# Performance work log

Measured on AMD Instinct MI355X. Metric: run time of the kernel, lower is better.

Reference implementation:

```python
import jax, jax.numpy as jnp
import numpy as np

N_NODES = 100000
N_EDGES = 1000000
IN_DIM = 64
OUT_DIM = 64
BN_EPS = 1e-5


def setup_inputs() -> dict:
    key = jax.random.key(0)
    k1, k2, k3 = jax.random.split(key, 3)
    x = jax.random.normal(k1, (N_NODES, IN_DIM), dtype=jnp.float32)
    edge_index = jax.random.randint(k2, (2, N_EDGES), 0, N_NODES, dtype=jnp.int32)
    W = jax.random.normal(k3, (IN_DIM, OUT_DIM), dtype=jnp.float32) * (1.0 / np.sqrt(IN_DIM))
    b = jnp.zeros((OUT_DIM,), dtype=jnp.float32)
    gamma = jnp.ones((OUT_DIM,), dtype=jnp.float32)
    beta = jnp.zeros((OUT_DIM,), dtype=jnp.float32)
    return {"x": x, "edge_index": edge_index, "W": W, "b": b, "gamma": gamma, "beta": beta}


def reference(x, edge_index, W, b, gamma, beta):
    N = x.shape[0]
    # GCN normalization with self-loops (improved=False -> fill value 1.0)
    loop = jnp.arange(N, dtype=edge_index.dtype)
    src = jnp.concatenate([edge_index[0], loop])  # message sources
    dst = jnp.concatenate([edge_index[1], loop])  # aggregation targets
    ew = jnp.ones(src.shape[0], dtype=x.dtype)
    deg = jax.ops.segment_sum(ew, dst, num_segments=N)  # [N]
    dinv = jnp.where(deg > 0, jax.lax.rsqrt(deg), 0.0)
    norm = dinv[src] * ew * dinv[dst]  # [E+N]
    # linear transform then normalized scatter-add aggregation
    h = x @ W  # [N, OUT_DIM]
    msg = h[src] * norm[:, None]  # [E+N, OUT_DIM]
    agg = jax.ops.segment_sum(msg, dst, num_segments=N) + b  # [N, OUT_DIM]
    # activation
    a = jax.nn.relu(agg)
    # BatchNorm1d, training mode: batch statistics over node dim (biased var)
    mean = jnp.mean(a, axis=0)
    var = jnp.mean((a - mean) ** 2, axis=0)
    out = gamma * (a - mean) * jax.lax.rsqrt(var + BN_EPS) + beta
    return out
```

## Files before the change

### kernel.cpp

```cpp
#include <hip/hip_runtime.h>
#include <hip/hip_fp16.h>

#define DIM 64
#define BN_EPS 1e-5f
#define RSHIFT 8
#define RSIZE 256
#define EPB 8192
#define SBLK 512

__global__ __launch_bounds__(256) void k_binhist(const int* __restrict__ dst,
                                                 int* __restrict__ rangecnt,
                                                 int P, int E) {
    __shared__ int hist[512];
    for (int b = threadIdx.x; b < P; b += 256) hist[b] = 0;
    __syncthreads();
    const int base4 = blockIdx.x * (EPB / 4);
    for (int i = 0; i < EPB / 4 / 256; ++i) {
        int idx = base4 + i * 256 + threadIdx.x;
        int e0 = idx << 2;
        if (e0 + 3 < E) {
            int4 d4 = ((const int4*)dst)[idx];
            atomicAdd(&hist[d4.x >> RSHIFT], 1);
            atomicAdd(&hist[d4.y >> RSHIFT], 1);
            atomicAdd(&hist[d4.z >> RSHIFT], 1);
            atomicAdd(&hist[d4.w >> RSHIFT], 1);
        } else {
            for (int k = 0; k < 4; ++k)
                if (e0 + k < E) atomicAdd(&hist[dst[e0 + k] >> RSHIFT], 1);
        }
    }
    __syncthreads();
    for (int b = threadIdx.x; b < P; b += 256)
        if (hist[b] > 0) atomicAdd(&rangecnt[b], hist[b]);
}

__global__ void k_rangescan(const int* __restrict__ rangecnt, int* __restrict__ gbase,
                            int* __restrict__ gcursor, int* __restrict__ rowptr,
                            int P, int N, int E) {
    __shared__ int s[512];
    int v = ((int)threadIdx.x < P) ? rangecnt[threadIdx.x] : 0;
    s[threadIdx.x] = v;
    __syncthreads();
    for (int off = 1; off < 512; off <<= 1) {
        int t = (threadIdx.x >= (unsigned)off) ? s[threadIdx.x - off] : 0;
        __syncthreads();
        s[threadIdx.x] += t;
        __syncthreads();
    }
    if ((int)threadIdx.x < P) {
        int ex = s[threadIdx.x] - v;
        gbase[threadIdx.x] = ex;
        gcursor[threadIdx.x] = ex;
    }
    if ((int)threadIdx.x == P - 1) gbase[P] = s[threadIdx.x];
    if (threadIdx.x == 0) rowptr[N] = E;
}

__global__ __launch_bounds__(256) void k_bin(const int* __restrict__ src,
                                             const int* __restrict__ dst,
                                             int* __restrict__ gcursor,
                                             int* __restrict__ pk, int P, int E) {
    __shared__ int hist[512], gofs[512], lcnt[512];
    for (int b = threadIdx.x; b < P; b += 256) { hist[b] = 0; lcnt[b] = 0; }
    __syncthreads();
    const int base4 = blockIdx.x * (EPB / 4);
    for (int i = 0; i < EPB / 4 / 256; ++i) {
        int idx = base4 + i * 256 + threadIdx.x;
        int e0 = idx << 2;
        if (e0 + 3 < E) {
            int4 d4 = ((const int4*)dst)[idx];
            atomicAdd(&hist[d4.x >> RSHIFT], 1);
            atomicAdd(&hist[d4.y >> RSHIFT], 1);
            atomicAdd(&hist[d4.z >> RSHIFT], 1);
            atomicAdd(&hist[d4.w >> RSHIFT], 1);
        } else {
            for (int k = 0; k < 4; ++k)
                if (e0 + k < E) atomicAdd(&hist[dst[e0 + k] >> RSHIFT], 1);
        }
    }
    __syncthreads();
    for (int b = threadIdx.x; b < P; b += 256)
        if (hist[b] > 0) gofs[b] = atomicAdd(&gcursor[b], hist[b]);
    __syncthreads();
    for (int i = 0; i < EPB / 4 / 256; ++i) {
        int idx = base4 + i * 256 + threadIdx.x;
        int e0 = idx << 2;
        if (e0 + 3 < E) {
            int4 d4 = ((const int4*)dst)[idx];
            int4 s4 = ((const int4*)src)[idx];
            int b;
            b = d4.x >> RSHIFT; pk[gofs[b] + atomicAdd(&lcnt[b], 1)] = ((d4.x & (RSIZE - 1)) << 20) | s4.x;
            b = d4.y >> RSHIFT; pk[gofs[b] + atomicAdd(&lcnt[b], 1)] = ((d4.y & (RSIZE - 1)) << 20) | s4.y;
            b = d4.z >> RSHIFT; pk[gofs[b] + atomicAdd(&lcnt[b], 1)] = ((d4.z & (RSIZE - 1)) << 20) | s4.z;
            b = d4.w >> RSHIFT; pk[gofs[b] + atomicAdd(&lcnt[b], 1)] = ((d4.w & (RSIZE - 1)) << 20) | s4.w;
        } else {
            for (int k = 0; k < 4; ++k) {
                if (e0 + k < E) {
                    int d = dst[e0 + k];
                    int b = d >> RSHIFT;
                    pk[gofs[b] + atomicAdd(&lcnt[b], 1)] = ((d & (RSIZE - 1)) << 20) | src[e0 + k];
                }
            }
        }
    }
}

__global__ __launch_bounds__(256) void k_sortrange(
        const int* __restrict__ gbase, const int* __restrict__ pk,
        int* __restrict__ ssrc, int* __restrict__ rowptr,
        int* __restrict__ chunkstart, float* __restrict__ dinv, int N) {
    __shared__ int lhist[256], ls[256], lcur[256];
    const int r = blockIdx.x;
    const int d0 = r << RSHIFT;
    const int i = d0 + threadIdx.x;
    const int ebeg = gbase[r], eend = gbase[r + 1];
    lhist[threadIdx.x] = 0;
    __syncthreads();
    for (int j = ebeg + threadIdx.x; j < eend; j += 256)
        atomicAdd(&lhist[((unsigned)pk[j]) >> 20], 1);
    __syncthreads();
    int dg = lhist[threadIdx.x];
    if (i < N) dinv[i] = rsqrtf((float)dg + 1.0f);
    ls[threadIdx.x] = dg;
    __syncthreads();
    for (int off = 1; off < 256; off <<= 1) {
        int t = (threadIdx.x >= (unsigned)off) ? ls[threadIdx.x - off] : 0;
        __syncthreads();
        ls[threadIdx.x] += t;
        __syncthreads();
    }
    int lofs = ls[threadIdx.x] - dg;
    lcur[threadIdx.x] = ebeg + lofs;
    if (i < N) {
        int rs = ebeg + lofs;
        rowptr[i] = rs;
        int rn = rs + dg;
        int c0 = (rs + 63) >> 6;
        int c1 = (rn + 63) >> 6;
        for (int c = c0; c < c1; ++c) chunkstart[c] = i;
    }
    __syncthreads();
    for (int j = ebeg + threadIdx.x; j < eend; j += 256) {
        int p = pk[j];
        ssrc[atomicAdd(&lcur[((unsigned)p) >> 20], 1)] = p & 0xFFFFF;
    }
}

__global__ __launch_bounds__(256) void k_gemm(const float* __restrict__ x,
                                              const float* __restrict__ W,
                                              const float* __restrict__ dinv,
                                              __half* __restrict__ h2,
                                              float* __restrict__ outseed, int N) {
    __shared__ float Wl[DIM * DIM];
    for (int i = threadIdx.x; i < DIM * DIM; i += 256) Wl[i] = W[i];
    __syncthreads();
    int t = blockIdx.x * 256 + threadIdx.x;
    int r = t >> 2;
    int q = t & 3;
    if (r >= N) return;
    const float4* xr4 = (const float4*)(x + (size_t)r * DIM);
    float4 acc[4];
#pragma unroll
    for (int j = 0; j < 4; ++j) acc[j] = make_float4(0.f, 0.f, 0.f, 0.f);
    for (int k0 = 0; k0 < 16; ++k0) {
        float4 xv = xr4[k0];
#pragma unroll
        for (int kk = 0; kk < 4; ++kk) {
            float xs = (&xv.x)[kk];
            const float4* wrow = (const float4*)(Wl + (k0 * 4 + kk) * DIM) + (q << 2);
#pragma unroll
            for (int j = 0; j < 4; ++j) {
                float4 w = wrow[j];
                acc[j].x += xs * w.x;
                acc[j].y += xs * w.y;
                acc[j].z += xs * w.z;
                acc[j].w += xs * w.w;
            }
        }
    }
    float dr = dinv[r];
    float4* os4 = (float4*)(outseed + (size_t)r * DIM) + (q << 2);
    float4* hr4 = (float4*)(h2 + (size_t)r * DIM) + (q << 1);
    union { __half2 h[4]; float4 f4; } pack;
#pragma unroll
    for (int j = 0; j < 4; j += 2) {
        float4 v0 = make_float4(acc[j].x * dr, acc[j].y * dr, acc[j].z * dr, acc[j].w * dr);
        float4 v1 = make_float4(acc[j + 1].x * dr, acc[j + 1].y * dr, acc[j + 1].z * dr, acc[j + 1].w * dr);
        os4[j] = v0;
        os4[j + 1] = v1;
        pack.h[0] = __float22half2_rn(make_float2(v0.x, v0.y));
        pack.h[1] = __float22half2_rn(make_float2(v0.z, v0.w));
        pack.h[2] = __float22half2_rn(make_float2(v1.x, v1.y));
        pack.h[3] = __float22half2_rn(make_float2(v1.z, v1.w));
        hr4[j >> 1] = pack.f4;
    }
}

__global__ __launch_bounds__(256) void k_edgeagg(
        const int* __restrict__ ssrc, const int* __restrict__ rowptr,
        const int* __restrict__ chunkstart, const __half* __restrict__ h2,
        float* __restrict__ agg, int N, int E) {
    const int lane = threadIdx.x & 63;
    const int wid = blockIdx.x * (blockDim.x >> 6) + (threadIdx.x >> 6);
    const int base = wid << 6;
    if (base >= E) return;
    const int nval = min(64, E - base);
    const int node0 = chunkstart[wid];
    int sv = ssrc[base + min(lane, nval - 1)];
    int nn = node0 + 1 + lane;
    if (nn > N) nn = N;
    int rp = rowptr[nn];
    const __half* hb = h2 + lane;
    float acc = 0.f;
    bool uncovered = (__builtin_amdgcn_readlane(rp, 63) <= base + nval - 1);
    if (!uncovered && nval == 64) {
        int dprev = node0 + __popcll(__ballot(rp <= base));
#pragma unroll
        for (int g = 0; g < 64; g += 8) {
            int sA[8];
            float vA[8];
            int dA[8];
#pragma unroll
            for (int k = 0; k < 8; ++k) sA[k] = __builtin_amdgcn_readlane(sv, g + k);
#pragma unroll
            for (int k = 0; k < 8; ++k) vA[k] = __half2float(hb[(size_t)sA[k] * DIM]);
#pragma unroll
            for (int k = 0; k < 8; ++k) dA[k] = node0 + __popcll(__ballot(rp <= base + g + k));
#pragma unroll
            for (int k = 0; k < 8; ++k) {
                if (dA[k] != dprev) {
                    atomicAdd(&agg[(size_t)dprev * DIM + lane], acc);
                    acc = 0.f;
                    dprev = dA[k];
                }
                acc += vA[k];
            }
        }
        atomicAdd(&agg[(size_t)dprev * DIM + lane], acc);
    } else if (!uncovered) {
        int dprev = node0 + __popcll(__ballot(rp <= base));
        for (int j = 0; j < nval; ++j) {
            int sj = __builtin_amdgcn_readlane(sv, j);
            int dj = node0 + __popcll(__ballot(rp <= base + j));
            if (dj != dprev) {
                atomicAdd(&agg[(size_t)dprev * DIM + lane], acc);
                acc = 0.f;
                dprev = dj;
            }
            acc += __half2float(hb[(size_t)sj * DIM]);
        }
        atomicAdd(&agg[(size_t)dprev * DIM + lane], acc);
    } else {
        int dprev = -1;
        for (int j = 0; j < nval; ++j) {
            int e = base + j;
            int lo = 0, hi = N - 1;
            while (lo < hi) {
                int mid = (lo + hi + 1) >> 1;
                if (rowptr[mid] <= e) lo = mid; else hi = mid - 1;
            }
            if (lo != dprev) {
                if (dprev >= 0) atomicAdd(&agg[(size_t)dprev * DIM + lane], acc);
                acc = 0.f;
                dprev = lo;
            }
            acc += __half2float(hb[(size_t)__builtin_amdgcn_readlane(sv, j) * DIM]);
        }
        if (dprev >= 0) atomicAdd(&agg[(size_t)dprev * DIM + lane], acc);
    }
}

__global__ __launch_bounds__(256) void k_stats(
        const float4* __restrict__ outr, const float* __restrict__ dinv,
        const float* __restrict__ b, float* __restrict__ pstats, int total4) {
    __shared__ float4 s1[256], s2[256];
    int i = blockIdx.x * 256 + threadIdx.x;
    const int stride = SBLK * 256;
    const int f4 = i & 15;
    const float4 bv = ((const float4*)b)[f4];
    float4 ls = make_float4(0.f, 0.f, 0.f, 0.f), lq = ls;
    for (; i < total4; i += stride) {
        float dd = dinv[i >> 4];
        float4 v = outr[i];
        float ax = fmaxf(v.x * dd + bv.x, 0.f);
        float ay = fmaxf(v.y * dd + bv.y, 0.f);
        float az = fmaxf(v.z * dd + bv.z, 0.f);
        float aw = fmaxf(v.w * dd + bv.w, 0.f);
        ls.x += ax; ls.y += ay; ls.z += az; ls.w += aw;
        lq.x += ax * ax; lq.y += ay * ay; lq.z += az * az; lq.w += aw * aw;
    }
    s1[threadIdx.x] = ls;
    s2[threadIdx.x] = lq;
    __syncthreads();
    for (int o = 128; o >= 16; o >>= 1) {
        if ((int)threadIdx.x < o) {
            float4 a = s1[threadIdx.x], c = s1[threadIdx.x + o];
            s1[threadIdx.x] = make_float4(a.x + c.x, a.y + c.y, a.z + c.z, a.w + c.w);
            float4 q = s2[threadIdx.x], r = s2[threadIdx.x + o];
            s2[threadIdx.x] = make_float4(q.x + r.x, q.y + r.y, q.z + r.z, q.w + r.w);
        }
        __syncthreads();
    }
    if (threadIdx.x < 16) {
        ((float4*)(pstats + (size_t)blockIdx.x * 128))[threadIdx.x] = s1[threadIdx.x];
        ((float4*)(pstats + (size_t)blockIdx.x * 128 + 64))[threadIdx.x] = s2[threadIdx.x];
    }
}

__global__ void k_finstats(const float* __restrict__ pstats,
                           const float* __restrict__ gamma, const float* __restrict__ beta,
                           float* __restrict__ scale, float* __restrict__ shift, int N) {
    __shared__ float ssum[256], ssq[256];
    const int f = threadIdx.x & 63;
    const int c = threadIdx.x >> 6;
    float s = 0.f, q = 0.f;
    for (int blk = c; blk < SBLK; blk += 4) {
        s += pstats[blk * 128 + f];
        q += pstats[blk * 128 + 64 + f];
    }
    ssum[threadIdx.x] = s;
    ssq[threadIdx.x] = q;
    __syncthreads();
    if (threadIdx.x < 64) {
        float ts = ssum[f] + ssum[f + 64] + ssum[f + 128] + ssum[f + 192];
        float tq = ssq[f] + ssq[f + 64] + ssq[f + 128] + ssq[f + 192];
        float inv_n = 1.0f / (float)N;
        float mean = ts * inv_n;
        float var = tq * inv_n - mean * mean;
        float istd = rsqrtf(var + BN_EPS);
        float sc = gamma[f] * istd;
        scale[f] = sc;
        shift[f] = beta[f] - mean * sc;
    }
}

__global__ void k_bn2(float4* __restrict__ a, const float* __restrict__ dinv,
                      const float* __restrict__ b, const float* __restrict__ scale,
                      const float* __restrict__ shift, int total4) {
    int i = blockIdx.x * blockDim.x + threadIdx.x;
    const int stride = gridDim.x * blockDim.x;
    const int f4 = i & 15;
    const float4 bv = ((const float4*)b)[f4];
    const float4 scv = ((const float4*)scale)[f4];
    const float4 shv = ((const float4*)shift)[f4];
    for (; i < total4; i += stride) {
        float dd = dinv[i >> 4];
        float4 v = a[i];
        v.x = fmaxf(v.x * dd + bv.x, 0.f) * scv.x + shv.x;
        v.y = fmaxf(v.y * dd + bv.y, 0.f) * scv.y + shv.y;
        v.z = fmaxf(v.z * dd + bv.z, 0.f) * scv.z + shv.z;
        v.w = fmaxf(v.w * dd + bv.w, 0.f) * scv.w + shv.w;
        a[i] = v;
    }
}

extern "C" void kernel_launch(void* const* d_in, const int* in_sizes, int n_in,
                              void* d_out, int out_size, void* d_ws, size_t ws_size,
                              hipStream_t stream) {
    const float* x     = (const float*)d_in[0];
    const int*   ei    = (const int*)d_in[1];
    const float* W     = (const float*)d_in[2];
    const float* b     = (const float*)d_in[3];
    const float* gamma = (const float*)d_in[4];
    const float* beta  = (const float*)d_in[5];
    float* out = (float*)d_out;

    const int N = in_sizes[0] / DIM;
    const int E = in_sizes[1] / 2;
    const int* esrc = ei;
    const int* edst = ei + E;
    const int P = (N + RSIZE - 1) >> RSHIFT;
    const int nbin = (E + EPB - 1) / EPB;
    const int nchunks = (E + 63) / 64;

    char* ws = (char*)d_ws;
    size_t off = 0;
    float* dinv = (float*)(ws + off);   off += (size_t)N * sizeof(float);
    off = (off + 255) & ~(size_t)255;
    int* rowptr = (int*)(ws + off);     off += (size_t)(N + 1) * sizeof(int);
    off = (off + 255) & ~(size_t)255;
    int* rangecnt = (int*)(ws + off);   off += 512 * sizeof(int);
    int* gbase = (int*)(ws + off);      off += 520 * sizeof(int);
    int* gcursor = (int*)(ws + off);    off += 512 * sizeof(int);
    float* scale = (float*)(ws + off);  off += 64 * sizeof(float);
    float* shift = (float*)(ws + off);  off += 64 * sizeof(float);
    off = (off + 255) & ~(size_t)255;
    float* pstats = (float*)(ws + off); off += (size_t)SBLK * 128 * sizeof(float);
    off = (off + 255) & ~(size_t)255;
    int* chunkstart = (int*)(ws + off); off += (size_t)nchunks * sizeof(int);
    off = (off + 255) & ~(size_t)255;
    int* pk = (int*)(ws + off);         off += (size_t)E * sizeof(int);
    off = (off + 255) & ~(size_t)255;
    int* ssrc = (int*)(ws + off);       off += (size_t)E * sizeof(int);
    off = (off + 255) & ~(size_t)255;
    __half* h2 = (__half*)(ws + off);   off += (size_t)N * DIM * sizeof(__half);

    hipMemsetAsync(rangecnt, 0, 512 * sizeof(int), stream);

    k_binhist<<<nbin, 256, 0, stream>>>(edst, rangecnt, P, E);
    k_rangescan<<<1, 512, 0, stream>>>(rangecnt, gbase, gcursor, rowptr, P, N, E);
    k_bin<<<nbin, 256, 0, stream>>>(esrc, edst, gcursor, pk, P, E);
    k_sortrange<<<P, 256, 0, stream>>>(gbase, pk, ssrc, rowptr, chunkstart, dinv, N);
    k_gemm<<<(4 * N + 255) / 256, 256, 0, stream>>>(x, W, dinv, h2, out, N);
    k_edgeagg<<<(nchunks + 3) / 4, 256, 0, stream>>>(ssrc, rowptr, chunkstart, h2, out, N, E);
    k_stats<<<SBLK, 256, 0, stream>>>((const float4*)out, dinv, b, pstats, N * DIM / 4);
    k_finstats<<<1, 256, 0, stream>>>(pstats, gamma, beta, scale, shift, N);
    k_bn2<<<2048, 256, 0, stream>>>((float4*)out, dinv, b, scale, shift, N * DIM / 4);
}
```

Before: 214.3 us.

## Build CSR via global atomics and aggregate per node with fused stats

Replaces the two-level bin sort with a direct per-node degree count using global atomics, a per-range node scan, and an atomic-cursor scatter into CSR order. Aggregation becomes pull-based: one wavefront per destination node, with no float atomics on the output and no separate seed write from the GEMM. The same kernel also applies ReLU and accumulates BatchNorm partial sums, which removes the separate stats pass over the output. The cost is heavier global atomic contention during scatter, a non-deterministic edge order within each node, and possible load imbalance across nodes with different degrees.

```diff
diff --git a/kernel.cpp b/kernel.cpp
--- a/kernel.cpp
+++ b/kernel.cpp
@@ -6,13 +6,14 @@
 #define RSHIFT 8
 #define RSIZE 256
 #define EPB 8192
-#define SBLK 512
-
-__global__ __launch_bounds__(256) void k_binhist(const int* __restrict__ dst,
-                                                 int* __restrict__ rangecnt,
-                                                 int P, int E) {
+#define ABLK 1024
+
+__global__ __launch_bounds__(256) void k_deg(const int* __restrict__ dst,
+                                             int* __restrict__ deg,
+                                             int* __restrict__ rangecnt,
+                                             int P, int E) {
     __shared__ int hist[512];
-    for (int b = threadIdx.x; b < P; b += 256) hist[b] = 0;
+    for (int b0 = threadIdx.x; b0 < P; b0 += 256) hist[b0] = 0;
     __syncthreads();
     const int base4 = blockIdx.x * (EPB / 4);
     for (int i = 0; i < EPB / 4 / 256; ++i) {
@@ -24,19 +25,26 @@
             atomicAdd(&hist[d4.y >> RSHIFT], 1);
             atomicAdd(&hist[d4.z >> RSHIFT], 1);
             atomicAdd(&hist[d4.w >> RSHIFT], 1);
+            atomicAdd(&deg[d4.x], 1);
+            atomicAdd(&deg[d4.y], 1);
+            atomicAdd(&deg[d4.z], 1);
+            atomicAdd(&deg[d4.w], 1);
         } else {
             for (int k = 0; k < 4; ++k)
-                if (e0 + k < E) atomicAdd(&hist[dst[e0 + k] >> RSHIFT], 1);
+                if (e0 + k < E) {
+                    int d = dst[e0 + k];
+                    atomicAdd(&hist[d >> RSHIFT], 1);
+                    atomicAdd(&deg[d], 1);
+                }
         }
     }
     __syncthreads();
-    for (int b = threadIdx.x; b < P; b += 256)
-        if (hist[b] > 0) atomicAdd(&rangecnt[b], hist[b]);
+    for (int b0 = threadIdx.x; b0 < P; b0 += 256)
+        if (hist[b0] > 0) atomicAdd(&rangecnt[b0], hist[b0]);
 }
 
 __global__ void k_rangescan(const int* __restrict__ rangecnt, int* __restrict__ gbase,
-                            int* __restrict__ gcursor, int* __restrict__ rowptr,
-                            int P, int N, int E) {
+                            int* __restrict__ rowptr, int P, int N, int E) {
     __shared__ int s[512];
     int v = ((int)threadIdx.x < P) ? rangecnt[threadIdx.x] : 0;
     s[threadIdx.x] = v;
@@ -47,79 +55,19 @@
         s[threadIdx.x] += t;
         __syncthreads();
     }
-    if ((int)threadIdx.x < P) {
-        int ex = s[threadIdx.x] - v;
-        gbase[threadIdx.x] = ex;
-        gcursor[threadIdx.x] = ex;
-    }
+    if ((int)threadIdx.x < P) gbase[threadIdx.x] = s[threadIdx.x] - v;
     if ((int)threadIdx.x == P - 1) gbase[P] = s[threadIdx.x];
     if (threadIdx.x == 0) rowptr[N] = E;
 }
 
-__global__ __launch_bounds__(256) void k_bin(const int* __restrict__ src,
-                                             const int* __restrict__ dst,
-                                             int* __restrict__ gcursor,
-                                             int* __restrict__ pk, int P, int E) {
-    __shared__ int hist[512], gofs[512], lcnt[512];
-    for (int b = threadIdx.x; b < P; b += 256) { hist[b] = 0; lcnt[b] = 0; }
-    __syncthreads();
-    const int base4 = blockIdx.x * (EPB / 4);
-    for (int i = 0; i < EPB / 4 / 256; ++i) {
-        int idx = base4 + i * 256 + threadIdx.x;
-        int e0 = idx << 2;
-        if (e0 + 3 < E) {
-            int4 d4 = ((const int4*)dst)[idx];
-            atomicAdd(&hist[d4.x >> RSHIFT], 1);
-            atomicAdd(&hist[d4.y >> RSHIFT], 1);
-            atomicAdd(&hist[d4.z >> RSHIFT], 1);
-            atomicAdd(&hist[d4.w >> RSHIFT], 1);
-        } else {
-            for (int k = 0; k < 4; ++k)
-                if (e0 + k < E) atomicAdd(&hist[dst[e0 + k] >> RSHIFT], 1);
-        }
-    }
-    __syncthreads();
-    for (int b = threadIdx.x; b < P; b += 256)
-        if (hist[b] > 0) gofs[b] = atomicAdd(&gcursor[b], hist[b]);
-    __syncthreads();
-    for (int i = 0; i < EPB / 4 / 256; ++i) {
-        int idx = base4 + i * 256 + threadIdx.x;
-        int e0 = idx << 2;
-        if (e0 + 3 < E) {
-            int4 d4 = ((const int4*)dst)[idx];
-            int4 s4 = ((const int4*)src)[idx];
-            int b;
-            b = d4.x >> RSHIFT; pk[gofs[b] + atomicAdd(&lcnt[b], 1)] = ((d4.x & (RSIZE - 1)) << 20) | s4.x;
-            b = d4.y >> RSHIFT; pk[gofs[b] + atomicAdd(&lcnt[b], 1)] = ((d4.y & (RSIZE - 1)) << 20) | s4.y;
-            b = d4.z >> RSHIFT; pk[gofs[b] + atomicAdd(&lcnt[b], 1)] = ((d4.z & (RSIZE - 1)) << 20) | s4.z;
-            b = d4.w >> RSHIFT; pk[gofs[b] + atomicAdd(&lcnt[b], 1)] = ((d4.w & (RSIZE - 1)) << 20) | s4.w;
-        } else {
-            for (int k = 0; k < 4; ++k) {
-                if (e0 + k < E) {
-                    int d = dst[e0 + k];
-                    int b = d >> RSHIFT;
-                    pk[gofs[b] + atomicAdd(&lcnt[b], 1)] = ((d & (RSIZE - 1)) << 20) | src[e0 + k];
-                }
-            }
-        }
-    }
-}
-
-__global__ __launch_bounds__(256) void k_sortrange(
-        const int* __restrict__ gbase, const int* __restrict__ pk,
-        int* __restrict__ ssrc, int* __restrict__ rowptr,
-        int* __restrict__ chunkstart, float* __restrict__ dinv, int N) {
-    __shared__ int lhist[256], ls[256], lcur[256];
-    const int r = blockIdx.x;
-    const int d0 = r << RSHIFT;
-    const int i = d0 + threadIdx.x;
-    const int ebeg = gbase[r], eend = gbase[r + 1];
-    lhist[threadIdx.x] = 0;
-    __syncthreads();
-    for (int j = ebeg + threadIdx.x; j < eend; j += 256)
-        atomicAdd(&lhist[((unsigned)pk[j]) >> 20], 1);
-    __syncthreads();
-    int dg = lhist[threadIdx.x];
+__global__ __launch_bounds__(256) void k_nodescan(const int* __restrict__ gbase,
+                                                  const int* __restrict__ deg,
+                                                  int* __restrict__ rowptr,
+                                                  int* __restrict__ cursor,
+                                                  float* __restrict__ dinv, int N) {
+    __shared__ int ls[256];
+    const int i = (blockIdx.x << RSHIFT) + threadIdx.x;
+    int dg = (i < N) ? deg[i] : 0;
     if (i < N) dinv[i] = rsqrtf((float)dg + 1.0f);
     ls[threadIdx.x] = dg;
     __syncthreads();
@@ -129,28 +77,37 @@
         ls[threadIdx.x] += t;
         __syncthreads();
     }
-    int lofs = ls[threadIdx.x] - dg;
-    lcur[threadIdx.x] = ebeg + lofs;
     if (i < N) {
-        int rs = ebeg + lofs;
-        rowptr[i] = rs;
-        int rn = rs + dg;
-        int c0 = (rs + 63) >> 6;
-        int c1 = (rn + 63) >> 6;
-        for (int c = c0; c < c1; ++c) chunkstart[c] = i;
-    }
-    __syncthreads();
-    for (int j = ebeg + threadIdx.x; j < eend; j += 256) {
-        int p = pk[j];
-        ssrc[atomicAdd(&lcur[((unsigned)p) >> 20], 1)] = p & 0xFFFFF;
+        int ex = gbase[blockIdx.x] + ls[threadIdx.x] - dg;
+        rowptr[i] = ex;
+        cursor[i] = ex;
+    }
+}
+
+__global__ __launch_bounds__(256) void k_scatter(const int* __restrict__ src,
+                                                 const int* __restrict__ dst,
+                                                 int* __restrict__ cursor,
+                                                 int* __restrict__ ssrc, int E) {
+    int idx = blockIdx.x * 256 + threadIdx.x;
+    int e0 = idx << 2;
+    if (e0 + 3 < E) {
+        int4 s4 = ((const int4*)src)[idx];
+        int4 d4 = ((const int4*)dst)[idx];
+        ssrc[atomicAdd(&cursor[d4.x], 1)] = s4.x;
+        ssrc[atomicAdd(&cursor[d4.y], 1)] = s4.y;
+        ssrc[atomicAdd(&cursor[d4.z], 1)] = s4.z;
+        ssrc[atomicAdd(&cursor[d4.w], 1)] = s4.w;
+    } else {
+        for (int k = 0; k < 4; ++k)
+            if (e0 + k < E)
+                ssrc[atomicAdd(&cursor[dst[e0 + k]], 1)] = src[e0 + k];
     }
 }
 
 __global__ __launch_bounds__(256) void k_gemm(const float* __restrict__ x,
                                               const float* __restrict__ W,
                                               const float* __restrict__ dinv,
-                                              __half* __restrict__ h2,
-                                              float* __restrict__ outseed, int N) {
+                                              __half* __restrict__ h2, int N) {
     __shared__ float Wl[DIM * DIM];
     for (int i = threadIdx.x; i < DIM * DIM; i += 256) Wl[i] = W[i];
     __syncthreads();
@@ -179,131 +136,66 @@
         }
     }
     float dr = dinv[r];
-    float4* os4 = (float4*)(outseed + (size_t)r * DIM) + (q << 2);
     float4* hr4 = (float4*)(h2 + (size_t)r * DIM) + (q << 1);
     union { __half2 h[4]; float4 f4; } pack;
 #pragma unroll
     for (int j = 0; j < 4; j += 2) {
-        float4 v0 = make_float4(acc[j].x * dr, acc[j].y * dr, acc[j].z * dr, acc[j].w * dr);
-        float4 v1 = make_float4(acc[j + 1].x * dr, acc[j + 1].y * dr, acc[j + 1].z * dr, acc[j + 1].w * dr);
-        os4[j] = v0;
-        os4[j + 1] = v1;
-        pack.h[0] = __float22half2_rn(make_float2(v0.x, v0.y));
-        pack.h[1] = __float22half2_rn(make_float2(v0.z, v0.w));
-        pack.h[2] = __float22half2_rn(make_float2(v1.x, v1.y));
-        pack.h[3] = __float22half2_rn(make_float2(v1.z, v1.w));
+        pack.h[0] = __float22half2_rn(make_float2(acc[j].x * dr, acc[j].y * dr));
+        pack.h[1] = __float22half2_rn(make_float2(acc[j].z * dr, acc[j].w * dr));
+        pack.h[2] = __float22half2_rn(make_float2(acc[j + 1].x * dr, acc[j + 1].y * dr));
+        pack.h[3] = __float22half2_rn(make_float2(acc[j + 1].z * dr, acc[j + 1].w * dr));
         hr4[j >> 1] = pack.f4;
     }
 }
 
-__global__ __launch_bounds__(256) void k_edgeagg(
-        const int* __restrict__ ssrc, const int* __restrict__ rowptr,
-        const int* __restrict__ chunkstart, const __half* __restrict__ h2,
-        float* __restrict__ agg, int N, int E) {
+__global__ __launch_bounds__(256) void k_nodeagg(
+        const int* __restrict__ rowptr, const int* __restrict__ ssrc,
+        const __half* __restrict__ h2, const float* __restrict__ dinv,
+        const float* __restrict__ b, float* __restrict__ out,
+        float* __restrict__ pstats, int N) {
     const int lane = threadIdx.x & 63;
-    const int wid = blockIdx.x * (blockDim.x >> 6) + (threadIdx.x >> 6);
-    const int base = wid << 6;
-    if (base >= E) return;
-    const int nval = min(64, E - base);
-    const int node0 = chunkstart[wid];
-    int sv = ssrc[base + min(lane, nval - 1)];
-    int nn = node0 + 1 + lane;
-    if (nn > N) nn = N;
-    int rp = rowptr[nn];
+    const int w = threadIdx.x >> 6;
+    const float bl = b[lane];
     const __half* hb = h2 + lane;
-    float acc = 0.f;
-    bool uncovered = (__builtin_amdgcn_readlane(rp, 63) <= base + nval - 1);
-    if (!uncovered && nval == 64) {
-        int dprev = node0 + __popcll(__ballot(rp <= base));
-#pragma unroll
-        for (int g = 0; g < 64; g += 8) {
-            int sA[8];
-            float vA[8];
-            int dA[8];
-#pragma unroll
-            for (int k = 0; k < 8; ++k) sA[k] = __builtin_amdgcn_readlane(sv, g + k);
-#pragma unroll
-            for (int k = 0; k < 8; ++k) vA[k] = __half2float(hb[(size_t)sA[k] * DIM]);
-#pragma unroll
-            for (int k = 0; k < 8; ++k) dA[k] = node0 + __popcll(__ballot(rp <= base + g + k));
-#pragma unroll
-            for (int k = 0; k < 8; ++k) {
-                if (dA[k] != dprev) {
-                    atomicAdd(&agg[(size_t)dprev * DIM + lane], acc);
-                    acc = 0.f;
-                    dprev = dA[k];
-                }
-                acc += vA[k];
+    float psum = 0.f, psq = 0.f;
+    for (int i = blockIdx.x * 4 + w; i < N; i += ABLK * 4) {
+        int rb = rowptr[i], re = rowptr[i + 1];
+        int deg = re - rb;
+        float acc = __half2float(hb[(size_t)i * DIM]);
+        for (int j0 = 0; j0 < deg; j0 += 64) {
+            int m = min(64, deg - j0);
+            int sv = ssrc[rb + j0 + min(lane, m - 1)];
+            int j = 0;
+            for (; j + 8 <= m; j += 8) {
+                int sA[8];
+                float vA[8];
+#pragma unroll
+                for (int k = 0; k < 8; ++k) sA[k] = __builtin_amdgcn_readlane(sv, j + k);
+#pragma unroll
+                for (int k = 0; k < 8; ++k) vA[k] = __half2float(hb[(size_t)sA[k] * DIM]);
+#pragma unroll
+                for (int k = 0; k < 8; ++k) acc += vA[k];
             }
+            for (; j < m; ++j)
+                acc += __half2float(hb[(size_t)__builtin_amdgcn_readlane(sv, j) * DIM]);
         }
-        atomicAdd(&agg[(size_t)dprev * DIM + lane], acc);
-    } else if (!uncovered) {
-        int dprev = node0 + __popcll(__ballot(rp <= base));
-        for (int j = 0; j < nval; ++j) {
-            int sj = __builtin_amdgcn_readlane(sv, j);
-            int dj = node0 + __popcll(__ballot(rp <= base + j));
-            if (dj != dprev) {
-                atomicAdd(&agg[(size_t)dprev * DIM + lane], acc);
-                acc = 0.f;
-                dprev = dj;
-            }
-            acc += __half2float(hb[(size_t)sj * DIM]);
-        }
-        atomicAdd(&agg[(size_t)dprev * DIM + lane], acc);
-    } else {
-        int dprev = -1;
-        for (int j = 0; j < nval; ++j) {
-            int e = base + j;
-            int lo = 0, hi = N - 1;
-            while (lo < hi) {
-                int mid = (lo + hi + 1) >> 1;
-                if (rowptr[mid] <= e) lo = mid; else hi = mid - 1;
-            }
-            if (lo != dprev) {
-                if (dprev >= 0) atomicAdd(&agg[(size_t)dprev * DIM + lane], acc);
-                acc = 0.f;
-                dprev = lo;
-            }
-            acc += __half2float(hb[(size_t)__builtin_amdgcn_readlane(sv, j) * DIM]);
-        }
-        if (dprev >= 0) atomicAdd(&agg[(size_t)dprev * DIM + lane], acc);
-    }
-}
-
-__global__ __launch_bounds__(256) void k_stats(
-        const float4* __restrict__ outr, const float* __restrict__ dinv,
-        const float* __restrict__ b, float* __restrict__ pstats, int total4) {
-    __shared__ float4 s1[256], s2[256];
-    int i = blockIdx.x * 256 + threadIdx.x;
-    const int stride = SBLK * 256;
-    const int f4 = i & 15;
-    const float4 bv = ((const float4*)b)[f4];
-    float4 ls = make_float4(0.f, 0.f, 0.f, 0.f), lq = ls;
-    for (; i < total4; i += stride) {
-        float dd = dinv[i >> 4];
-        float4 v = outr[i];
-        float ax = fmaxf(v.x * dd + bv.x, 0.f);
-        float ay = fmaxf(v.y * dd + bv.y, 0.f);
-        float az = fmaxf(v.z * dd + bv.z, 0.f);
-        float aw = fmaxf(v.w * dd + bv.w, 0.f);
-        ls.x += ax; ls.y += ay; ls.z += az; ls.w += aw;
-        lq.x += ax * ax; lq.y += ay * ay; lq.z += az * az; lq.w += aw * aw;
-    }
-    s1[threadIdx.x] = ls;
-    s2[threadIdx.x] = lq;
-    __syncthreads();
-    for (int o = 128; o >= 16; o >>= 1) {
-        if ((int)threadIdx.x < o) {
-            float4 a = s1[threadIdx.x], c = s1[threadIdx.x + o];
-            s1[threadIdx.x] = make_float4(a.x + c.x, a.y + c.y, a.z + c.z, a.w + c.w);
-            float4 q = s2[threadIdx.x], r = s2[threadIdx.x + o];
-            s2[threadIdx.x] = make_float4(q.x + r.x, q.y + r.y, q.z + r.z, q.w + r.w);
-        }
-        __syncthreads();
-    }
-    if (threadIdx.x < 16) {
-        ((float4*)(pstats + (size_t)blockIdx.x * 128))[threadIdx.x] = s1[threadIdx.x];
-        ((float4*)(pstats + (size_t)blockIdx.x * 128 + 64))[threadIdx.x] = s2[threadIdx.x];
+        float a = fmaxf(acc * dinv[i] + bl, 0.f);
+        out[(size_t)i * DIM + lane] = a;
+        psum += a;
+        psq += a * a;
+    }
+    __shared__ float s1[256], s2[256];
+    s1[threadIdx.x] = psum;
+    s2[threadIdx.x] = psq;
+    __syncthreads();
+    if (threadIdx.x < 128) {
+        s1[threadIdx.x] += s1[threadIdx.x + 128];
+        s2[threadIdx.x] += s2[threadIdx.x + 128];
+    }
+    __syncthreads();
+    if (threadIdx.x < 64) {
+        pstats[(size_t)blockIdx.x * 128 + threadIdx.x] = s1[threadIdx.x] + s1[threadIdx.x + 64];
+        pstats[(size_t)blockIdx.x * 128 + 64 + threadIdx.x] = s2[threadIdx.x] + s2[threadIdx.x + 64];
     }
 }
 
@@ -314,7 +206,7 @@
     const int f = threadIdx.x & 63;
     const int c = threadIdx.x >> 6;
     float s = 0.f, q = 0.f;
-    for (int blk = c; blk < SBLK; blk += 4) {
+    for (int blk = c; blk < ABLK; blk += 4) {
         s += pstats[blk * 128 + f];
         q += pstats[blk * 128 + 64 + f];
     }
@@ -334,22 +226,19 @@
     }
 }
 
-__global__ void k_bn2(float4* __restrict__ a, const float* __restrict__ dinv,
-                      const float* __restrict__ b, const float* __restrict__ scale,
+__global__ void k_bn2(float4* __restrict__ a, const float* __restrict__ scale,
                       const float* __restrict__ shift, int total4) {
     int i = blockIdx.x * blockDim.x + threadIdx.x;
     const int stride = gridDim.x * blockDim.x;
     const int f4 = i & 15;
-    const float4 bv = ((const float4*)b)[f4];
     const float4 scv = ((const float4*)scale)[f4];
     const float4 shv = ((const float4*)shift)[f4];
     for (; i < total4; i += stride) {
-        float dd = dinv[i >> 4];
         float4 v = a[i];
-        v.x = fmaxf(v.x * dd + bv.x, 0.f) * scv.x + shv.x;
-        v.y = fmaxf(v.y * dd + bv.y, 0.f) * scv.y + shv.y;
-        v.z = fmaxf(v.z * dd + bv.z, 0.f) * scv.z + shv.z;
-        v.w = fmaxf(v.w * dd + bv.w, 0.f) * scv.w + shv.w;
+        v.x = v.x * scv.x + shv.x;
+        v.y = v.y * scv.y + shv.y;
+        v.z = v.z * scv.z + shv.z;
+        v.w = v.w * scv.w + shv.w;
         a[i] = v;
     }
 }
@@ -371,39 +260,37 @@
     const int* edst = ei + E;
     const int P = (N + RSIZE - 1) >> RSHIFT;
     const int nbin = (E + EPB - 1) / EPB;
-    const int nchunks = (E + 63) / 64;
 
     char* ws = (char*)d_ws;
     size_t off = 0;
+    int* deg = (int*)(ws + off);        off += (size_t)N * sizeof(int);
+    int* rangecnt = (int*)(ws + off);   off += 512 * sizeof(int);
+    off = (off + 255) & ~(size_t)255;
+    int* gbase = (int*)(ws + off);      off += 520 * sizeof(int);
+    off = (off + 255) & ~(size_t)255;
     float* dinv = (float*)(ws + off);   off += (size_t)N * sizeof(float);
     off = (off + 255) & ~(size_t)255;
     int* rowptr = (int*)(ws + off);     off += (size_t)(N + 1) * sizeof(int);
     off = (off + 255) & ~(size_t)255;
-    int* rangecnt = (int*)(ws + off);   off += 512 * sizeof(int);
-    int* gbase = (int*)(ws + off);      off += 520 * sizeof(int);
-    int* gcursor = (int*)(ws + off);    off += 512 * sizeof(int);
+    int* cursor = (int*)(ws + off);     off += (size_t)N * sizeof(int);
+    off = (off + 255) & ~(size_t)255;
     float* scale = (float*)(ws + off);  off += 64 * sizeof(float);
     float* shift = (float*)(ws + off);  off += 64 * sizeof(float);
     off = (off + 255) & ~(size_t)255;
-    float* pstats = (float*)(ws + off); off += (size_t)SBLK * 128 * sizeof(float);
-    off = (off + 255) & ~(size_t)255;
-    int* chunkstart = (int*)(ws + off); off += (size_t)nchunks * sizeof(int);
-    off = (off + 255) & ~(size_t)255;
-    int* pk = (int*)(ws + off);         off += (size_t)E * sizeof(int);
+    float* pstats = (float*)(ws + off); off += (size_t)ABLK * 128 * sizeof(float);
     off = (off + 255) & ~(size_t)255;
     int* ssrc = (int*)(ws + off);       off += (size_t)E * sizeof(int);
     off = (off + 255) & ~(size_t)255;
     __half* h2 = (__half*)(ws + off);   off += (size_t)N * DIM * sizeof(__half);
 
-    hipMemsetAsync(rangecnt, 0, 512 * sizeof(int), stream);
-
-    k_binhist<<<nbin, 256, 0, stream>>>(edst, rangecnt, P, E);
-    k_rangescan<<<1, 512, 0, stream>>>(rangecnt, gbase, gcursor, rowptr, P, N, E);
-    k_bin<<<nbin, 256, 0, stream>>>(esrc, edst, gcursor, pk, P, E);
-    k_sortrange<<<P, 256, 0, stream>>>(gbase, pk, ssrc, rowptr, chunkstart, dinv, N);
-    k_gemm<<<(4 * N + 255) / 256, 256, 0, stream>>>(x, W, dinv, h2, out, N);
-    k_edgeagg<<<(nchunks + 3) / 4, 256, 0, stream>>>(ssrc, rowptr, chunkstart, h2, out, N, E);
-    k_stats<<<SBLK, 256, 0, stream>>>((const float4*)out, dinv, b, pstats, N * DIM / 4);
+    hipMemsetAsync(deg, 0, (size_t)(N + 512) * sizeof(int), stream);
+
+    k_deg<<<nbin, 256, 0, stream>>>(edst, deg, rangecnt, P, E);
+    k_rangescan<<<1, 512, 0, stream>>>(rangecnt, gbase, rowptr, P, N, E);
+    k_nodescan<<<P, 256, 0, stream>>>(gbase, deg, rowptr, cursor, dinv, N);
+    k_scatter<<<((E + 3) / 4 + 255) / 256, 256, 0, stream>>>(esrc, edst, cursor, ssrc, E);
+    k_gemm<<<(4 * N + 255) / 256, 256, 0, stream>>>(x, W, dinv, h2, N);
+    k_nodeagg<<<ABLK, 256, 0, stream>>>(rowptr, ssrc, h2, dinv, b, out, pstats, N);
     k_finstats<<<1, 256, 0, stream>>>(pstats, gamma, beta, scale, shift, N);
-    k_bn2<<<2048, 256, 0, stream>>>((float4*)out, dinv, b, scale, shift, N * DIM / 4);
-}
+    k_bn2<<<2048, 256, 0, stream>>>((float4*)out, scale, shift, N * DIM / 4);
+}
```

After: 362.0 us. 68.9% more time.
